# Kernel optimization log

Hardware: AMD Instinct MI355X
Metric: run time of the kernel (lower is better)

## Reference

```python
import jax, jax.numpy as jnp
import numpy as np
import math

B, S, D = 2, 2048, 1024
N_HEAD = 16
EPS = 1e-6

def setup_inputs() -> dict:
    key = jax.random.key(0)
    ks = jax.random.split(key, 12)
    def lin(k):
        kw, kb = jax.random.split(k)
        scale = 1.0 / math.sqrt(D)
        W = jax.random.uniform(kw, (D, D), jnp.float32, -scale, scale)
        b = jax.random.uniform(kb, (D,), jnp.float32, -scale, scale)
        return W, b
    Wq, bq = lin(ks[0]); Wk, bk = lin(ks[1]); Wv, bv = lin(ks[2]); Wo, bo = lin(ks[3])
    return {
        'query': jax.random.normal(ks[4], (B, S, D), jnp.float32),
        'key':   jax.random.normal(ks[5], (B, S, D), jnp.float32),
        'value': jax.random.normal(ks[6], (B, S, D), jnp.float32),
        'mask':  jnp.ones((B, S, S), jnp.int32),
        'Wq': Wq, 'bq': bq, 'Wk': Wk, 'bk': bk, 'Wv': Wv, 'bv': bv,
        'Wo': Wo, 'bo': bo,
        'gamma': jnp.ones((D,), jnp.float32),
        'beta':  jnp.zeros((D,), jnp.float32),
    }

def reference(query, key, value, mask, Wq, bq, Wk, bk, Wv, bv, Wo, bo, gamma, beta):
    b, s, dm = query.shape
    h = N_HEAD
    d = dm // h
    residual = query
    # projections (torch Linear: x @ W.T + b) -> [b, h, s, d]
    def proj(x, W, bias):
        return (x @ W.T + bias).reshape(b, -1, h, d).transpose(0, 2, 1, 3)
    q = proj(query, Wq, bq)
    k = proj(key, Wk, bk)
    v = proj(value, Wv, bv)
    scores = jnp.einsum('bhqd,bhkd->bhqk', q, k) / jnp.sqrt(jnp.float32(d))
    scores = jnp.where(mask[:, None, :, :] == 0, jnp.float32(-1e9), scores)
    p_attn = jax.nn.softmax(scores, axis=-1)  # dropout is identity in eval/reference
    x = jnp.einsum('bhqk,bhkd->bhqd', p_attn, v)
    x = x.transpose(0, 2, 1, 3).reshape(b, -1, h * d)
    x = x @ Wo.T + bo
    x = x + residual
    # LayerNorm with unbiased std and (std + eps) denominator, as in source
    mean = jnp.mean(x, axis=-1, keepdims=True)
    std = jnp.std(x, axis=-1, keepdims=True, ddof=1)
    return gamma * (x - mean) / (std + EPS) + beta
```

## Files before the change

kernel.cpp:

```cpp
#include <hip/hip_runtime.h>
#include <hip/hip_bf16.h>
#include <math.h>
#include <stdint.h>

#define BATCH 2
#define SEQ   2048
#define DMODEL 1024
#define NHEAD 16
#define HDIM  64
#define NROWS (BATCH*SEQ)
#define EPS   1e-6f
#define QSCALE 0.1803368801111204f

typedef float f32x4 __attribute__((ext_vector_type(4)));
typedef short s16x8 __attribute__((ext_vector_type(8)));
typedef unsigned int u32x4 __attribute__((ext_vector_type(4)));

#define OFF_XQ 0
#define OFF_XK 4194304
#define OFF_XV 8388608
#define OFF_WQ 12582912
#define OFF_WK 13631488
#define OFF_WV 14680064
#define OFF_WO 15728640
#define OFF_QB 16777216
#define OFF_KB 20971520
#define OFF_VT 25165824
#define OFF_CM 29360128
#define OFF_MS 29884416

__device__ __forceinline__ unsigned short f2bf(float x) {
    unsigned int u = __builtin_bit_cast(unsigned int, x);
    u += 0x7fff + ((u >> 16) & 1);
    return (unsigned short)(u >> 16);
}

__device__ __forceinline__ void gl_lds16(const void* g, void* l) {
    __builtin_amdgcn_global_load_lds(
        (const __attribute__((address_space(1))) unsigned int*)g,
        (__attribute__((address_space(3))) unsigned int*)(unsigned int)(unsigned long long)l,
        16, 0, 0);
}

__global__ __launch_bounds__(256) void conv_all_kernel(
    const float* __restrict__ q, const float* __restrict__ k, const float* __restrict__ v,
    const float* __restrict__ wq, const float* __restrict__ wk, const float* __restrict__ wv,
    const float* __restrict__ wo, unsigned short* __restrict__ ws)
{
    if (blockIdx.x == 0 && threadIdx.x < 32)
        ((unsigned int*)(ws + OFF_MS))[threadIdx.x] = 0;
    size_t t = ((size_t)blockIdx.x * 256 + threadIdx.x) * 4;
    const float* src; unsigned short* dst; size_t off;
    if (t < 4194304)       { src = q;  dst = ws + OFF_XQ; off = t; }
    else if (t < 8388608)  { src = k;  dst = ws + OFF_XK; off = t - 4194304; }
    else if (t < 12582912) { src = v;  dst = ws + OFF_XV; off = t - 8388608; }
    else if (t < 13631488) { src = wq; dst = ws + OFF_WQ; off = t - 12582912; }
    else if (t < 14680064) { src = wk; dst = ws + OFF_WK; off = t - 13631488; }
    else if (t < 15728640) { src = wv; dst = ws + OFF_WV; off = t - 14680064; }
    else                   { src = wo; dst = ws + OFF_WO; off = t - 15728640; }
    float4 x = *(const float4*)&src[off];
    ushort4 o;
    o.x = f2bf(x.x); o.y = f2bf(x.y); o.z = f2bf(x.z); o.w = f2bf(x.w);
    *(ushort4*)&dst[off] = o;
}

__global__ __launch_bounds__(256) void mask_compress_kernel(
    const int* __restrict__ mask, unsigned long long* __restrict__ cm,
    unsigned int* __restrict__ msum)
{
    int t = blockIdx.x * 256 + threadIdx.x;
    int s  = t & 2047;
    int kb = (t >> 11) & 31;
    int b  = t >> 16;
    const int* mp = mask + ((size_t)b * SEQ + s) * SEQ + kb * 64;
    unsigned long long bits = 0;
    #pragma unroll
    for (int i = 0; i < 16; i++) {
        int4 m4 = *(const int4*)&mp[i * 4];
        unsigned long long nib =
            (unsigned long long)((m4.x != 0) | ((m4.y != 0) << 1) |
                                 ((m4.z != 0) << 2) | ((m4.w != 0) << 3));
        bits |= nib << (i * 4);
    }
    cm[((size_t)b * 32 + kb) * SEQ + s] = bits;
    if (bits != ~0ull)
        atomicOr(&msum[(b << 4) | (s >> 7)], 1u << kb);
}

__device__ __forceinline__ void gemm_body(
    const unsigned short* A, const unsigned short* W, int r0, int c0,
    unsigned short* As, unsigned short* Bs, f32x4 acc[4][4])
{
    const int tid  = threadIdx.x;
    const int wave = tid >> 6, lane = tid & 63;
    const int quad = lane >> 4, l15 = lane & 15;
    const int wr = wave >> 1, wc = wave & 1;
    for (int k0 = 0; k0 < DMODEL; k0 += 64) {
        __syncthreads();
        #pragma unroll
        for (int r = 0; r < 4; r++) {
            int f   = r * 4096 + tid * 16;
            int row = f >> 7;
            int g   = (((f >> 4) & 7) - row) & 7;
            gl_lds16((const char*)A + (size_t)(r0 + row) * 2048 + k0 * 2 + g * 16,
                     (char*)As + r * 4096 + wave * 1024);
            gl_lds16((const char*)W + (size_t)(c0 + row) * 2048 + k0 * 2 + g * 16,
                     (char*)Bs + r * 4096 + wave * 1024);
        }
        __syncthreads();
        #pragma unroll
        for (int ks = 0; ks < 2; ks++) {
            s16x8 a[4], b[4];
            #pragma unroll
            for (int mt = 0; mt < 4; mt++) {
                int row = wr*64 + mt*16 + l15;
                a[mt] = *(const s16x8*)((const char*)As + row * 128 + ((ks*4 + quad + row) & 7) * 16);
            }
            #pragma unroll
            for (int nt = 0; nt < 4; nt++) {
                int row = wc*64 + nt*16 + l15;
                b[nt] = *(const s16x8*)((const char*)Bs + row * 128 + ((ks*4 + quad + row) & 7) * 16);
            }
            #pragma unroll
            for (int mt = 0; mt < 4; mt++)
                #pragma unroll
                for (int nt = 0; nt < 4; nt++)
                    acc[mt][nt] = __builtin_amdgcn_mfma_f32_16x16x32_bf16(a[mt], b[nt], acc[mt][nt], 0, 0, 0);
        }
    }
}

__global__ __launch_bounds__(256) void qkv_gemm_kernel(
    unsigned short* __restrict__ ws,
    const float* __restrict__ bq, const float* __restrict__ bk, const float* __restrict__ bv)
{
    __shared__ __align__(16) unsigned short As[8192];
    __shared__ __align__(16) unsigned short Bs[8192];
    const int z = blockIdx.z;
    const unsigned short *A, *W;
    int r0, c0;
    if (z != 2) {
        A = ws + (size_t)z * 4194304;
        W = ws + OFF_WQ + (size_t)z * 1048576;
        r0 = blockIdx.x * 128; c0 = blockIdx.y * 128;
    } else {
        A = ws + OFF_WV;
        W = ws + OFF_XV;
        r0 = blockIdx.y * 128; c0 = blockIdx.x * 128;
    }
    const float* bias = (z == 0) ? bq : (z == 1 ? bk : bv);
    unsigned short* outp = ws + OFF_QB + (size_t)z * 4194304;
    const float scale = (z == 0) ? QSCALE : 1.0f;

    f32x4 acc[4][4] = {};
    gemm_body(A, W, r0, c0, As, Bs, acc);

    const int lane = threadIdx.x & 63, wave = threadIdx.x >> 6;
    const int quad = lane >> 4, l15 = lane & 15;
    const int wr = wave >> 1, wc = wave & 1;
    if (z != 2) {
        float bias_v[4];
        #pragma unroll
        for (int nt = 0; nt < 4; nt++) bias_v[nt] = bias[c0 + wc*64 + nt*16 + l15];
        #pragma unroll
        for (int mt = 0; mt < 4; mt++) {
            #pragma unroll
            for (int nt = 0; nt < 4; nt++) {
                int c = c0 + wc*64 + nt*16 + l15;
                int hh = c >> 6, dd = c & 63;
                #pragma unroll
                for (int reg = 0; reg < 4; reg++) {
                    int r = r0 + wr*64 + mt*16 + quad*4 + reg;
                    int bb = r >> 11, ss = r & (SEQ - 1);
                    float val = (acc[mt][nt][reg] + bias_v[nt]) * scale;
                    outp[(((size_t)(bb*NHEAD + hh)) * SEQ + ss) * HDIM + dd] = f2bf(val);
                }
            }
        }
    } else {
        #pragma unroll
        for (int mt = 0; mt < 4; mt++) {
            #pragma unroll
            for (int reg = 0; reg < 4; reg++) {
                int f = r0 + wr*64 + mt*16 + quad*4 + reg;
                int hh = f >> 6, dd = f & 63;
                float bfv = bias[f];
                #pragma unroll
                for (int nt = 0; nt < 4; nt++) {
                    int r = c0 + wc*64 + nt*16 + l15;
                    int bb = r >> 11, ss = r & (SEQ - 1);
                    outp[(((size_t)(bb*NHEAD + hh)) * HDIM + dd) * SEQ + ss] =
                        f2bf(acc[mt][nt][reg] + bfv);
                }
            }
        }
    }
}

__global__ __launch_bounds__(256) void oproj_gemm_kernel(
    const unsigned short* __restrict__ ws, const float* __restrict__ bo,
    const float* __restrict__ resid, float* __restrict__ outf)
{
    __shared__ __align__(16) unsigned short As[8192];
    __shared__ __align__(16) unsigned short Bs[8192];
    const unsigned short* A = ws + OFF_XQ;
    const unsigned short* W = ws + OFF_WO;
    const int r0 = blockIdx.x * 128, c0 = blockIdx.y * 128;

    f32x4 acc[4][4] = {};
    gemm_body(A, W, r0, c0, (unsigned short*)As, (unsigned short*)Bs, acc);

    const int lane = threadIdx.x & 63, wave = threadIdx.x >> 6;
    const int quad = lane >> 4, l15 = lane & 15;
    const int wr = wave >> 1, wc = wave & 1;
    #pragma unroll
    for (int mt = 0; mt < 4; mt++) {
        #pragma unroll
        for (int nt = 0; nt < 4; nt++) {
            int c = c0 + wc*64 + nt*16 + l15;
            float bv = bo[c];
            #pragma unroll
            for (int reg = 0; reg < 4; reg++) {
                int r = r0 + wr*64 + mt*16 + quad*4 + reg;
                size_t idx = (size_t)r * DMODEL + c;
                outf[idx] = acc[mt][nt][reg] + bv + resid[idx];
            }
        }
    }
}

__global__ __launch_bounds__(512) void attn_mfma_kernel(
    const unsigned short* __restrict__ ws,
    const unsigned long long* __restrict__ cmask,
    const unsigned int* __restrict__ msum,
    unsigned short* __restrict__ ab)
{
    const int tid  = threadIdx.x;
    const int wave = tid >> 6, lane = tid & 63;
    const int quad = lane >> 4, l15 = lane & 15;
    const int h = blockIdx.y, b = blockIdx.z;
    const int qw = blockIdx.x * 128 + wave * 16;

    const char* qh = (const char*)(ws + OFF_QB + ((size_t)(b*NHEAD + h)) * SEQ * HDIM);
    const char* kh = (const char*)(ws + OFF_KB + ((size_t)(b*NHEAD + h)) * SEQ * HDIM);
    const char* vh = (const char*)(ws + OFF_VT + ((size_t)(b*NHEAD + h)) * SEQ * HDIM);

    __shared__ __align__(16) char Ks[2][8192];
    __shared__ __align__(16) char Vs[2][8192];

    const unsigned int chunkflags = msum[(b << 4) | blockIdx.x];

    const int srow = tid >> 3;
    const int sgrp = ((tid & 7) - srow) & 7;
    const int arow = (srow & 0x23) | ((srow & 0x0C) << 1) | ((srow & 0x10) >> 2);

    #define STAGE(bf, k0)                                                       \
        do {                                                                    \
            gl_lds16(kh + (size_t)((k0) + arow) * 128 + sgrp * 16,              \
                     Ks[bf] + wave * 1024);                                     \
            gl_lds16(vh + (size_t)srow * 4096 + (size_t)(k0) * 2 + sgrp * 16,   \
                     Vs[bf] + wave * 1024);                                     \
        } while (0)

    s16x8 qa[2];
    #pragma unroll
    for (int ks = 0; ks < 2; ks++)
        qa[ks] = *(const s16x8*)(qh + (size_t)(qw + l15) * 128 + ks*64 + quad*16);

    int koff[4][2], voff[4][2];
    #pragma unroll
    for (int kt = 0; kt < 4; kt++) {
        int prow = kt*16 + l15;
        koff[kt][0] = prow*128 + ((quad     + prow) & 7) * 16;
        koff[kt][1] = prow*128 + ((4 + quad + prow) & 7) * 16;
    }
    #pragma unroll
    for (int nt = 0; nt < 4; nt++) {
        int d = nt*16 + l15;
        voff[nt][0] = d*128 + ((quad     + d) & 7) * 16;
        voff[nt][1] = d*128 + ((4 + quad + d) & 7) * 16;
    }

    s16x8 onesf;
    {
        short so = (short)0x3F80;
        if (l15 == 0) onesf = (s16x8){so, so, so, so, so, so, so, so};
        else          onesf = (s16x8){0, 0, 0, 0, 0, 0, 0, 0};
    }

    f32x4 o[4], lsum = {0.f, 0.f, 0.f, 0.f};
    #pragma unroll
    for (int nt = 0; nt < 4; nt++) o[nt] = (f32x4){0.f, 0.f, 0.f, 0.f};

    STAGE(0, 0);
    int bf = 0;
    for (int k0 = 0; k0 < SEQ; k0 += 64) {
        __syncthreads();
        if (k0 + 64 < SEQ) STAGE(bf ^ 1, k0 + 64);

        const char* Kb = Ks[bf];
        const char* Vb = Vs[bf];
        f32x4 st[4];
        #pragma unroll
        for (int kt = 0; kt < 4; kt++) {
            s16x8 kf0 = *(const s16x8*)(Kb + koff[kt][0]);
            s16x8 kf1 = *(const s16x8*)(Kb + koff[kt][1]);
            f32x4 z = {0.f, 0.f, 0.f, 0.f};
            st[kt] = __builtin_amdgcn_mfma_f32_16x16x32_bf16(kf0, qa[0], z, 0, 0, 0);
            st[kt] = __builtin_amdgcn_mfma_f32_16x16x32_bf16(kf1, qa[1], st[kt], 0, 0, 0);
        }
        if (chunkflags & (1u << (k0 >> 6))) {
            unsigned long long cm =
                cmask[((size_t)b*32 + (k0 >> 6)) * SEQ + qw + l15];
            if (cm != ~0ull) {
                #pragma unroll
                for (int kt = 0; kt < 4; kt++)
                    #pragma unroll
                    for (int reg = 0; reg < 4; reg++) {
                        int key = (kt >> 1)*32 + quad*8 + (kt & 1)*4 + reg;
                        if (!((cm >> key) & 1)) st[kt][reg] = -1e9f;
                    }
            }
        }
        #pragma unroll
        for (int ks = 0; ks < 2; ks++) {
            unsigned int pb[8];
            #pragma unroll
            for (int j = 0; j < 8; j++) {
                int kt = 2*ks + (j >> 2), r = j & 3;
                pb[j] = __builtin_bit_cast(unsigned int, exp2f(st[kt][r]));
            }
            u32x4 pw;
            pw[0] = __builtin_amdgcn_perm(pb[1], pb[0], 0x07060302u);
            pw[1] = __builtin_amdgcn_perm(pb[3], pb[2], 0x07060302u);
            pw[2] = __builtin_amdgcn_perm(pb[5], pb[4], 0x07060302u);
            pw[3] = __builtin_amdgcn_perm(pb[7], pb[6], 0x07060302u);
            s16x8 pa = __builtin_bit_cast(s16x8, pw);
            lsum = __builtin_amdgcn_mfma_f32_16x16x32_bf16(pa, onesf, lsum, 0, 0, 0);
            #pragma unroll
            for (int nt = 0; nt < 4; nt++) {
                s16x8 vf = *(const s16x8*)(Vb + voff[nt][ks]);
                o[nt] = __builtin_amdgcn_mfma_f32_16x16x32_bf16(pa, vf, o[nt], 0, 0, 0);
            }
        }
        bf ^= 1;
    }
    #undef STAGE
    #pragma unroll
    for (int reg = 0; reg < 4; reg++) {
        float lv = __shfl(lsum[reg], lane & 48);
        float inv = 1.f / lv;
        int sg = qw + quad*4 + reg;
        #pragma unroll
        for (int nt = 0; nt < 4; nt++) {
            size_t idx = ((size_t)b * SEQ + sg) * DMODEL + h*HDIM + nt*16 + l15;
            ab[idx] = f2bf(o[nt][reg] * inv);
        }
    }
}

__global__ __launch_bounds__(256) void ln_kernel(
    float* __restrict__ x, const float* __restrict__ gamma,
    const float* __restrict__ beta)
{
    const int row = blockIdx.x;
    const int tid = threadIdx.x;
    float4 vals = *(const float4*)&x[(size_t)row * DMODEL + tid * 4];
    float s  = vals.x + vals.y + vals.z + vals.w;
    float ss = vals.x*vals.x + vals.y*vals.y + vals.z*vals.z + vals.w*vals.w;
    #pragma unroll
    for (int off = 32; off > 0; off >>= 1) {
        s  += __shfl_down(s, off);
        ss += __shfl_down(ss, off);
    }
    __shared__ float sbuf[4], ssbuf[4];
    __shared__ float mean_s, inv_s;
    if ((tid & 63) == 0) { sbuf[tid >> 6] = s; ssbuf[tid >> 6] = ss; }
    __syncthreads();
    if (tid == 0) {
        float S1 = 0.f, S2 = 0.f;
        #pragma unroll
        for (int i = 0; i < 4; i++) { S1 += sbuf[i]; S2 += ssbuf[i]; }
        float mean = S1 * (1.0f / DMODEL);
        float var  = (S2 - (float)DMODEL * mean * mean) * (1.0f / (DMODEL - 1));
        float sd   = sqrtf(fmaxf(var, 0.f));
        mean_s = mean;
        inv_s  = 1.f / (sd + EPS);
    }
    __syncthreads();
    float4 g  = *(const float4*)&gamma[tid * 4];
    float4 bt = *(const float4*)&beta[tid * 4];
    float4 o;
    o.x = g.x * (vals.x - mean_s) * inv_s + bt.x;
    o.y = g.y * (vals.y - mean_s) * inv_s + bt.y;
    o.z = g.z * (vals.z - mean_s) * inv_s + bt.z;
    o.w = g.w * (vals.w - mean_s) * inv_s + bt.w;
    *(float4*)&x[(size_t)row * DMODEL + tid * 4] = o;
}

extern "C" void kernel_launch(void* const* d_in, const int* in_sizes, int n_in,
                              void* d_out, int out_size, void* d_ws, size_t ws_size,
                              hipStream_t stream) {
    const float* query = (const float*)d_in[0];
    const float* key   = (const float*)d_in[1];
    const float* value = (const float*)d_in[2];
    const int*   mask  = (const int*)d_in[3];
    const float* Wq = (const float*)d_in[4];  const float* bq = (const float*)d_in[5];
    const float* Wk = (const float*)d_in[6];  const float* bk = (const float*)d_in[7];
    const float* Wv = (const float*)d_in[8];  const float* bv = (const float*)d_in[9];
    const float* Wo = (const float*)d_in[10]; const float* bo = (const float*)d_in[11];
    const float* gamma = (const float*)d_in[12];
    const float* beta  = (const float*)d_in[13];
    float* out = (float*)d_out;

    unsigned short* ws = (unsigned short*)d_ws;
    unsigned long long* cmask = (unsigned long long*)(ws + OFF_CM);
    unsigned int* msum = (unsigned int*)(ws + OFF_MS);

    conv_all_kernel<<<16384, 256, 0, stream>>>(query, key, value, Wq, Wk, Wv, Wo, ws);
    mask_compress_kernel<<<512, 256, 0, stream>>>(mask, cmask, msum);
    qkv_gemm_kernel<<<dim3(32, 8, 3), 256, 0, stream>>>(ws, bq, bk, bv);
    attn_mfma_kernel<<<dim3(SEQ/128, NHEAD, BATCH), 512, 0, stream>>>(ws, cmask, msum, ws + OFF_XQ);
    oproj_gemm_kernel<<<dim3(32, 8), 256, 0, stream>>>(ws, bo, query, out);
    ln_kernel<<<NROWS, 256, 0, stream>>>(out, gamma, beta);
}
```

Before: 275.1 us.

## Ballot-based mask compression and 128-key attention staging per barrier

The mask compression kernel now gives each key block to a whole wavefront: each lane loads one int and the 64-bit mask comes from __ballot. This replaces per-thread strided int4 loops with coalesced loads over more blocks. The attention kernel stages two 64-key K/V tiles per double-buffer slot and processes 128 keys per loop iteration, which halves barrier count at the cost of doubling LDS use to 64KB per block. That may reduce occupancy.

```diff
diff --git a/kernel.cpp b/kernel.cpp
--- a/kernel.cpp
+++ b/kernel.cpp
@@ -69,22 +69,18 @@
     unsigned int* __restrict__ msum)
 {
     int t = blockIdx.x * 256 + threadIdx.x;
-    int s  = t & 2047;
-    int kb = (t >> 11) & 31;
-    int b  = t >> 16;
-    const int* mp = mask + ((size_t)b * SEQ + s) * SEQ + kb * 64;
-    unsigned long long bits = 0;
-    #pragma unroll
-    for (int i = 0; i < 16; i++) {
-        int4 m4 = *(const int4*)&mp[i * 4];
-        unsigned long long nib =
-            (unsigned long long)((m4.x != 0) | ((m4.y != 0) << 1) |
-                                 ((m4.z != 0) << 2) | ((m4.w != 0) << 3));
-        bits |= nib << (i * 4);
-    }
-    cm[((size_t)b * 32 + kb) * SEQ + s] = bits;
-    if (bits != ~0ull)
-        atomicOr(&msum[(b << 4) | (s >> 7)], 1u << kb);
+    int lane = t & 63;
+    int w = t >> 6;
+    int s  = w & 2047;
+    int kb = (w >> 11) & 31;
+    int b  = w >> 16;
+    int m = mask[((size_t)b * SEQ + s) * SEQ + kb * 64 + lane];
+    unsigned long long bits = __ballot(m != 0);
+    if (lane == 0) {
+        cm[((size_t)b * 32 + kb) * SEQ + s] = bits;
+        if (bits != ~0ull)
+            atomicOr(&msum[(b << 4) | (s >> 7)], 1u << kb);
+    }
 }
 
 __device__ __forceinline__ void gemm_body(
@@ -245,8 +241,8 @@
     const char* kh = (const char*)(ws + OFF_KB + ((size_t)(b*NHEAD + h)) * SEQ * HDIM);
     const char* vh = (const char*)(ws + OFF_VT + ((size_t)(b*NHEAD + h)) * SEQ * HDIM);
 
-    __shared__ __align__(16) char Ks[2][8192];
-    __shared__ __align__(16) char Vs[2][8192];
+    __shared__ __align__(16) char Ks[2][2][8192];
+    __shared__ __align__(16) char Vs[2][2][8192];
 
     const unsigned int chunkflags = msum[(b << 4) | blockIdx.x];
 
@@ -254,12 +250,16 @@
     const int sgrp = ((tid & 7) - srow) & 7;
     const int arow = (srow & 0x23) | ((srow & 0x0C) << 1) | ((srow & 0x10) >> 2);
 
-    #define STAGE(bf, k0)                                                       \
-        do {                                                                    \
-            gl_lds16(kh + (size_t)((k0) + arow) * 128 + sgrp * 16,              \
-                     Ks[bf] + wave * 1024);                                     \
-            gl_lds16(vh + (size_t)srow * 4096 + (size_t)(k0) * 2 + sgrp * 16,   \
-                     Vs[bf] + wave * 1024);                                     \
+    #define STAGE(bfi, k0)                                                           \
+        do {                                                                         \
+            gl_lds16(kh + (size_t)((k0) + arow) * 128 + sgrp * 16,                   \
+                     Ks[bfi][0] + wave * 1024);                                      \
+            gl_lds16(kh + (size_t)((k0) + 64 + arow) * 128 + sgrp * 16,              \
+                     Ks[bfi][1] + wave * 1024);                                      \
+            gl_lds16(vh + (size_t)srow * 4096 + (size_t)(k0) * 2 + sgrp * 16,        \
+                     Vs[bfi][0] + wave * 1024);                                      \
+            gl_lds16(vh + (size_t)srow * 4096 + (size_t)((k0) + 64) * 2 + sgrp * 16, \
+                     Vs[bfi][1] + wave * 1024);                                      \
         } while (0)
 
     s16x8 qa[2];
@@ -294,53 +294,57 @@
 
     STAGE(0, 0);
     int bf = 0;
-    for (int k0 = 0; k0 < SEQ; k0 += 64) {
+    for (int k0 = 0; k0 < SEQ; k0 += 128) {
         __syncthreads();
-        if (k0 + 64 < SEQ) STAGE(bf ^ 1, k0 + 64);
-
-        const char* Kb = Ks[bf];
-        const char* Vb = Vs[bf];
-        f32x4 st[4];
-        #pragma unroll
-        for (int kt = 0; kt < 4; kt++) {
-            s16x8 kf0 = *(const s16x8*)(Kb + koff[kt][0]);
-            s16x8 kf1 = *(const s16x8*)(Kb + koff[kt][1]);
-            f32x4 z = {0.f, 0.f, 0.f, 0.f};
-            st[kt] = __builtin_amdgcn_mfma_f32_16x16x32_bf16(kf0, qa[0], z, 0, 0, 0);
-            st[kt] = __builtin_amdgcn_mfma_f32_16x16x32_bf16(kf1, qa[1], st[kt], 0, 0, 0);
-        }
-        if (chunkflags & (1u << (k0 >> 6))) {
-            unsigned long long cm =
-                cmask[((size_t)b*32 + (k0 >> 6)) * SEQ + qw + l15];
-            if (cm != ~0ull) {
+        if (k0 + 128 < SEQ) STAGE(bf ^ 1, k0 + 128);
+
+        #pragma unroll
+        for (int half = 0; half < 2; half++) {
+            const char* Kb = Ks[bf][half];
+            const char* Vb = Vs[bf][half];
+            const int kc = (k0 >> 6) + half;
+            f32x4 st[4];
+            #pragma unroll
+            for (int kt = 0; kt < 4; kt++) {
+                s16x8 kf0 = *(const s16x8*)(Kb + koff[kt][0]);
+                s16x8 kf1 = *(const s16x8*)(Kb + koff[kt][1]);
+                f32x4 z = {0.f, 0.f, 0.f, 0.f};
+                st[kt] = __builtin_amdgcn_mfma_f32_16x16x32_bf16(kf0, qa[0], z, 0, 0, 0);
+                st[kt] = __builtin_amdgcn_mfma_f32_16x16x32_bf16(kf1, qa[1], st[kt], 0, 0, 0);
+            }
+            if (chunkflags & (1u << kc)) {
+                unsigned long long cm =
+                    cmask[((size_t)b*32 + kc) * SEQ + qw + l15];
+                if (cm != ~0ull) {
+                    #pragma unroll
+                    for (int kt = 0; kt < 4; kt++)
+                        #pragma unroll
+                        for (int reg = 0; reg < 4; reg++) {
+                            int key = (kt >> 1)*32 + quad*8 + (kt & 1)*4 + reg;
+                            if (!((cm >> key) & 1)) st[kt][reg] = -1e9f;
+                        }
+                }
+            }
+            #pragma unroll
+            for (int ks = 0; ks < 2; ks++) {
+                unsigned int pb[8];
                 #pragma unroll
-                for (int kt = 0; kt < 4; kt++)
-                    #pragma unroll
-                    for (int reg = 0; reg < 4; reg++) {
-                        int key = (kt >> 1)*32 + quad*8 + (kt & 1)*4 + reg;
-                        if (!((cm >> key) & 1)) st[kt][reg] = -1e9f;
-                    }
-            }
-        }
-        #pragma unroll
-        for (int ks = 0; ks < 2; ks++) {
-            unsigned int pb[8];
-            #pragma unroll
-            for (int j = 0; j < 8; j++) {
-                int kt = 2*ks + (j >> 2), r = j & 3;
-                pb[j] = __builtin_bit_cast(unsigned int, exp2f(st[kt][r]));
-            }
-            u32x4 pw;
-            pw[0] = __builtin_amdgcn_perm(pb[1], pb[0], 0x07060302u);
-            pw[1] = __builtin_amdgcn_perm(pb[3], pb[2], 0x07060302u);
-            pw[2] = __builtin_amdgcn_perm(pb[5], pb[4], 0x07060302u);
-            pw[3] = __builtin_amdgcn_perm(pb[7], pb[6], 0x07060302u);
-            s16x8 pa = __builtin_bit_cast(s16x8, pw);
-            lsum = __builtin_amdgcn_mfma_f32_16x16x32_bf16(pa, onesf, lsum, 0, 0, 0);
-            #pragma unroll
-            for (int nt = 0; nt < 4; nt++) {
-                s16x8 vf = *(const s16x8*)(Vb + voff[nt][ks]);
-                o[nt] = __builtin_amdgcn_mfma_f32_16x16x32_bf16(pa, vf, o[nt], 0, 0, 0);
+                for (int j = 0; j < 8; j++) {
+                    int kt = 2*ks + (j >> 2), r = j & 3;
+                    pb[j] = __builtin_bit_cast(unsigned int, exp2f(st[kt][r]));
+                }
+                u32x4 pw;
+                pw[0] = __builtin_amdgcn_perm(pb[1], pb[0], 0x07060302u);
+                pw[1] = __builtin_amdgcn_perm(pb[3], pb[2], 0x07060302u);
+                pw[2] = __builtin_amdgcn_perm(pb[5], pb[4], 0x07060302u);
+                pw[3] = __builtin_amdgcn_perm(pb[7], pb[6], 0x07060302u);
+                s16x8 pa = __builtin_bit_cast(s16x8, pw);
+                lsum = __builtin_amdgcn_mfma_f32_16x16x32_bf16(pa, onesf, lsum, 0, 0, 0);
+                #pragma unroll
+                for (int nt = 0; nt < 4; nt++) {
+                    s16x8 vf = *(const s16x8*)(Vb + voff[nt][ks]);
+                    o[nt] = __builtin_amdgcn_mfma_f32_16x16x32_bf16(pa, vf, o[nt], 0, 0, 0);
+                }
             }
         }
         bf ^= 1;
@@ -418,7 +422,7 @@
     unsigned int* msum = (unsigned int*)(ws + OFF_MS);
 
     conv_all_kernel<<<16384, 256, 0, stream>>>(query, key, value, Wq, Wk, Wv, Wo, ws);
-    mask_compress_kernel<<<512, 256, 0, stream>>>(mask, cmask, msum);
+    mask_compress_kernel<<<32768, 256, 0, stream>>>(mask, cmask, msum);
     qkv_gemm_kernel<<<dim3(32, 8, 3), 256, 0, stream>>>(ws, bq, bk, bv);
     attn_mfma_kernel<<<dim3(SEQ/128, NHEAD, BATCH), 512, 0, stream>>>(ws, cmask, msum, ws + OFF_XQ);
     oproj_gemm_kernel<<<dim3(32, 8), 256, 0, stream>>>(ws, bo, query, out);
```

New measurement: 283.2 us. 2.9% more time.
